# Optimization experiments

Hardware: AMD Instinct MI355X
Metric: run time of the kernel (lower is better)

The kernel has to match this reference:

```python
import jax, jax.numpy as jnp
import numpy as np

EPS = 1e-6
NUM_HEADS = 16
ROPE_THETA = 100000.0


def _rope_tables(seq_len, head_dim, theta):
    inv_freq = 1.0 / (theta ** (np.arange(0, head_dim, 2, dtype=np.float32) / head_dim))
    t = np.arange(seq_len, dtype=np.float32)
    freqs = np.outer(t, inv_freq)                      # (S, head_dim//2)
    emb = np.concatenate([freqs, freqs], axis=-1)      # (S, head_dim)
    return jnp.asarray(np.cos(emb))[None], jnp.asarray(np.sin(emb))[None]  # (1,S,D)


def setup_inputs() -> dict:
    key = jax.random.key(0)
    ks = jax.random.split(key, 6)
    B, S, H = 2, 2048, 1024
    head_dim = H // NUM_HEADS
    cos, sin = _rope_tables(S, head_dim, ROPE_THETA)
    scale = 0.02
    return {
        "hidden_states": jax.random.normal(ks[0], (B, S, H), dtype=jnp.float32),
        "cos": cos, "sin": sin,
        "Wq": jax.random.normal(ks[1], (H, H), dtype=jnp.float32) * scale,
        "bq": jnp.zeros((H,), dtype=jnp.float32),
        "Wk": jax.random.normal(ks[2], (H, H), dtype=jnp.float32) * scale,
        "bk": jnp.zeros((H,), dtype=jnp.float32),
        "Wv": jax.random.normal(ks[3], (H, H), dtype=jnp.float32) * scale,
        "bv": jnp.zeros((H,), dtype=jnp.float32),
        "Wo": jax.random.normal(ks[4], (H, H), dtype=jnp.float32) * scale,
        "bo": jnp.zeros((H,), dtype=jnp.float32),
        "rms_weight": jnp.ones((H,), dtype=jnp.float32),
    }


def _rms_norm(x, w):
    var = jnp.mean(x * x, axis=-1, keepdims=True)
    return x * jax.lax.rsqrt(var + EPS) * w


def _rotate_half(x):
    x1, x2 = jnp.split(x, 2, axis=-1)
    return jnp.concatenate([-x2, x1], axis=-1)


def reference(hidden_states, cos, sin, Wq, bq, Wk, bk, Wv, bv, Wo, bo, rms_weight):
    B, S, H = hidden_states.shape
    D = H // NUM_HEADS
    q = hidden_states @ Wq.T + bq
    k = hidden_states @ Wk.T + bk
    v = hidden_states @ Wv.T + bv
    # RMSNorm over full hidden dim BEFORE head split (as in original)
    q = _rms_norm(q, rms_weight)
    k = _rms_norm(k, rms_weight)
    # (B,S,H) -> (B,heads,S,D)
    q = q.reshape(B, S, NUM_HEADS, D).transpose(0, 2, 1, 3)
    k = k.reshape(B, S, NUM_HEADS, D).transpose(0, 2, 1, 3)
    v = v.reshape(B, S, NUM_HEADS, D).transpose(0, 2, 1, 3)
    # RoPE: cos/sin (1,S,D) -> unsqueeze head dim
    c = cos[:, None, :, :]
    s = sin[:, None, :, :]
    q = q * c + _rotate_half(q) * s
    k = k * c + _rotate_half(k) * s
    # attention (faithful: boolean tril mask is ADDED as 0/1, not -inf)
    scale = D ** 0.5
    scores = jnp.einsum("bhqd,bhkd->bhqk", q, k) / scale
    mask = jnp.tril(jnp.ones((S, S), dtype=scores.dtype))  # +1 on causal, +0 elsewhere
    attn = jax.nn.softmax(scores + mask, axis=-1)
    out = jnp.einsum("bhqk,bhkd->bhqd", attn, v)
    out = out.transpose(0, 2, 1, 3).reshape(B, S, H)
    return out @ Wo.T + bo
```

## Files before the change

kernel.cpp:

```cpp
#include <hip/hip_runtime.h>

typedef unsigned short u16;
typedef __attribute__((ext_vector_type(8))) short bf16x8;
typedef __attribute__((ext_vector_type(4))) short bf16x4;
typedef __attribute__((ext_vector_type(4))) float f32x4;

#define MFMA16(A,B,C) __builtin_amdgcn_mfma_f32_16x16x32_bf16(A,B,C,0,0,0)

__device__ __forceinline__ u16 f2bf(float f){
  unsigned int u; __builtin_memcpy(&u,&f,4);
  unsigned int r = (u + 0x7fffu + ((u>>16)&1u)) >> 16;
  return (u16)r;
}
__device__ __forceinline__ float bf2f(u16 h){
  unsigned int u = ((unsigned int)h) << 16;
  float f; __builtin_memcpy(&f,&u,4); return f;
}

__device__ __forceinline__ void async_ld16(const void* g, void* l) {
  __builtin_amdgcn_global_load_lds(
      (const __attribute__((address_space(1))) unsigned int*)g,
      (__attribute__((address_space(3))) unsigned int*)l, 16, 0, 0);
}

__global__ __launch_bounds__(256) void cast_all(const float* __restrict__ hs,
    const float* __restrict__ wq, const float* __restrict__ wk,
    const float* __restrict__ wv, const float* __restrict__ wo,
    u16* __restrict__ dst)
{
  unsigned int i = blockIdx.x*256 + threadIdx.x;
  size_t el = (size_t)i * 8;
  const float* src; size_t off;
  if (el < 4194304) { src = hs; off = el; }
  else {
    unsigned int r = (unsigned int)((el - 4194304) >> 20);
    src = (r==0)?wq:(r==1)?wk:(r==2)?wv:wo;
    off = (el - 4194304) & 1048575;
  }
  float4 a = *reinterpret_cast<const float4*>(src+off);
  float4 b = *reinterpret_cast<const float4*>(src+off+4);
  u16 tmp[8] = {f2bf(a.x),f2bf(a.y),f2bf(a.z),f2bf(a.w),
                f2bf(b.x),f2bf(b.y),f2bf(b.z),f2bf(b.w)};
  *reinterpret_cast<uint4*>(dst + el) = *reinterpret_cast<const uint4*>(tmp);
}

template<int MODE>
__global__ __launch_bounds__(256) void gemm_k(const u16* __restrict__ A,
                                              const u16* __restrict__ W,
                                              const float* __restrict__ b0p,
                                              const float* __restrict__ b1p,
                                              const float* __restrict__ b2p,
                                              void* __restrict__ out,
                                              int M, int N, int K)
{
  __shared__ __align__(16) u16 lds_a[128*32];
  __shared__ __align__(16) u16 lds_w[128*32];
  const int t = threadIdx.x;
  const int lane = t & 63, wave = t >> 6;
  const int wm = wave >> 1, wn = wave & 1;
  const int lr = lane & 15, quad = lane >> 4;
  const int n0 = blockIdx.x * 128, m0 = blockIdx.y * 128;
  const int wbase = t & 192;

  const f32x4 fzero = {0.f,0.f,0.f,0.f};
  f32x4 acc[4][4];
  #pragma unroll
  for (int i=0;i<4;++i)
    #pragma unroll
    for (int j=0;j<4;++j) acc[i][j] = fzero;

  for (int k0 = 0; k0 < K; k0 += 32) {
    __syncthreads();
    #pragma unroll
    for (int it=0; it<2; ++it) {
      int idx = it*256 + t;
      int row = idx >> 2, c8 = (idx & 3) * 8;
      int lbase = (it*256 + wbase) * 8;
      async_ld16(&A[(size_t)(m0+row)*K + k0 + c8], &lds_a[lbase]);
      async_ld16(&W[(size_t)(n0+row)*K + k0 + c8], &lds_w[lbase]);
    }
    __syncthreads();
    bf16x8 af[4], bfr[4];
    #pragma unroll
    for (int mt=0; mt<4; ++mt)
      af[mt] = *reinterpret_cast<const bf16x8*>(&lds_a[(wm*64 + mt*16 + lr)*32 + quad*8]);
    #pragma unroll
    for (int nt=0; nt<4; ++nt)
      bfr[nt] = *reinterpret_cast<const bf16x8*>(&lds_w[(wn*64 + nt*16 + lr)*32 + quad*8]);
    #pragma unroll
    for (int mt=0; mt<4; ++mt)
      #pragma unroll
      for (int nt=0; nt<4; ++nt)
        acc[mt][nt] = MFMA16(af[mt], bfr[nt], acc[mt][nt]);
  }

  if (MODE == 0) {
    float* O = reinterpret_cast<float*>(out);
    #pragma unroll
    for (int nt=0; nt<4; ++nt) {
      int n = n0 + wn*64 + nt*16 + lr;
      float bv = b0p[n];
      #pragma unroll
      for (int mt=0; mt<4; ++mt)
        #pragma unroll
        for (int r=0; r<4; ++r) {
          int m = m0 + wm*64 + mt*16 + quad*4 + r;
          O[(size_t)m * N + n] = acc[mt][nt][r] + bv;
        }
    }
  } else {
    int which = n0 >> 10;
    const float* bp = (which==0) ? b0p : (which==1) ? b1p : b2p;
    u16* dst = reinterpret_cast<u16*>(out) + (size_t)which * 4194304;
    if (which == 2) {
      #pragma unroll
      for (int nt=0; nt<4; ++nt) {
        int nn = (n0 & 1023) + wn*64 + nt*16 + lr;
        float bv = bp[nn];
        int hh = nn >> 6, d = nn & 63;
        #pragma unroll
        for (int mt=0; mt<4; ++mt) {
          int m = m0 + wm*64 + mt*16 + quad*4;
          int b = m >> 11, s = m & 2047;
          u16 o[4];
          #pragma unroll
          for (int r=0; r<4; ++r) o[r] = f2bf(acc[mt][nt][r] + bv);
          *reinterpret_cast<uint2*>(&dst[((size_t)(b*16 + hh)*64 + d)*2048 + s]) =
              *reinterpret_cast<const uint2*>(o);
        }
      }
    } else {
      #pragma unroll
      for (int nt=0; nt<4; ++nt) {
        int nn = (n0 & 1023) + wn*64 + nt*16 + lr;
        float bv = bp[nn];
        int hh = nn >> 6, d = nn & 63;
        #pragma unroll
        for (int mt=0; mt<4; ++mt)
          #pragma unroll
          for (int r=0; r<4; ++r) {
            int m = m0 + wm*64 + mt*16 + quad*4 + r;
            int b = m >> 11, s = m & 2047;
            dst[((size_t)(b*16 + hh) * 2048 + s) * 64 + d] = f2bf(acc[mt][nt][r] + bv);
          }
      }
    }
  }
}

__global__ __launch_bounds__(256) void rmsrope(u16* __restrict__ qb, u16* __restrict__ kb,
                                               const float* __restrict__ cosb,
                                               const float* __restrict__ sinb,
                                               const float* __restrict__ w)
{
  u16* buf = blockIdx.y ? kb : qb;
  const int bs = blockIdx.x;
  const int b = bs >> 11, s = bs & 2047;
  const int t = threadIdx.x;
  float x1[2], x2[2];
  float ss = 0.f;
  #pragma unroll
  for (int i=0;i<2;++i){
    int p = t + i*256;
    int h = p >> 5, d = p & 31;
    size_t base = ((size_t)(b*16+h)*2048 + s)*64;
    x1[i] = bf2f(buf[base + d]);
    x2[i] = bf2f(buf[base + d + 32]);
    ss += x1[i]*x1[i] + x2[i]*x2[i];
  }
  #pragma unroll
  for (int off=32; off>0; off>>=1) ss += __shfl_xor(ss, off, 64);
  __shared__ float red[4];
  if ((t & 63) == 0) red[t>>6] = ss;
  __syncthreads();
  float tot = red[0]+red[1]+red[2]+red[3];
  float r = rsqrtf(tot * (1.0f/1024.0f) + 1e-6f);
  #pragma unroll
  for (int i=0;i<2;++i){
    int p = t + i*256;
    int h = p >> 5, d = p & 31;
    size_t base = ((size_t)(b*16+h)*2048 + s)*64;
    float w1 = w[h*64+d], w2 = w[h*64+d+32];
    float n1 = x1[i]*r*w1, n2 = x2[i]*r*w2;
    float c1 = cosb[s*64+d],    s1 = sinb[s*64+d];
    float c2 = cosb[s*64+d+32], s2 = sinb[s*64+d+32];
    buf[base+d]    = f2bf(n1*c1 - n2*s1);
    buf[base+d+32] = f2bf(n2*c2 + n1*s2);
  }
}

__global__ __launch_bounds__(256) void attn(const u16* __restrict__ qh,
                                            const u16* __restrict__ kh,
                                            const u16* __restrict__ vt,
                                            u16* __restrict__ ao)
{
  __shared__ __align__(16) u16 kbuf[64*64];
  __shared__ __align__(16) u16 vbuf[64*64];
  const int t = threadIdx.x;
  const int lane = t & 63, w = t >> 6;
  const int lr = lane & 15, quad = lane >> 4;
  const int qbase = blockIdx.x * 64;
  const int bh = blockIdx.y;
  const int b = bh >> 4, h = bh & 15;
  const size_t hb = (size_t)bh * 2048 * 64;
  const u16* qp = qh + hb;
  const u16* kp = kh + hb;
  const u16* vtp = vt + hb;

  const int q_abs = qbase + w*16 + lr;
  bf16x8 qf0 = *reinterpret_cast<const bf16x8*>(&qp[(size_t)q_abs*64 + quad*8]);
  bf16x8 qf1 = *reinterpret_cast<const bf16x8*>(&qp[(size_t)q_abs*64 + 32 + quad*8]);

  const f32x4 fzero = {0.f,0.f,0.f,0.f};
  f32x4 oacc[4];
  #pragma unroll
  for (int i=0;i<4;++i) oacc[i] = fzero;
  float lsum = 0.f;

  for (int kt=0; kt<32; ++kt) {
    __syncthreads();
    #pragma unroll
    for (int it=0; it<2; ++it) {
      int idx = it*256 + t;
      int row = idx >> 3, c = idx & 7;
      uint4 kvv = *reinterpret_cast<const uint4*>(&kp[(size_t)(kt*64+row)*64 + c*8]);
      uint4 vvv = *reinterpret_cast<const uint4*>(&vtp[(size_t)row*2048 + kt*64 + c*8]);
      int sw = ((c ^ (row&7))&7)*8;
      *reinterpret_cast<uint4*>(&kbuf[row*64 + sw]) = kvv;
      *reinterpret_cast<uint4*>(&vbuf[row*64 + sw]) = vvv;
    }
    __syncthreads();

    bf16x8 pfr[2];
    #pragma unroll
    for (int u=0; u<2; ++u) {
      bf16x4 ph[2];
      #pragma unroll
      for (int sidx=0; sidx<2; ++sidx) {
        int ksub = u*2 + sidx;
        int row = ksub*16 + lr, sw = row & 7;
        bf16x8 a0 = *reinterpret_cast<const bf16x8*>(&kbuf[row*64 + ((quad ^ sw)&7)*8]);
        bf16x8 a1 = *reinterpret_cast<const bf16x8*>(&kbuf[row*64 + ((quad ^ sw ^ 4)&7)*8]);
        f32x4 z = fzero;
        z = MFMA16(a0, qf0, z);
        z = MFMA16(a1, qf1, z);
        int key0 = kt*64 + ksub*16 + quad*4;
        u16 pp[4];
        #pragma unroll
        for (int r=0; r<4; ++r) {
          float sc = z[r]*0.125f + ((key0 + r <= q_abs) ? 1.0f : 0.0f);
          float p = __expf(sc);
          lsum += p;
          pp[r] = f2bf(p);
        }
        __builtin_memcpy(&ph[sidx], pp, 8);
      }
      pfr[u] = __builtin_shufflevector(ph[0], ph[1], 0,1,2,3,4,5,6,7);
    }

    #pragma unroll
    for (int u=0; u<2; ++u) {
      #pragma unroll
      for (int dt=0; dt<4; ++dt) {
        int row = dt*16 + lr, sw = row & 7;
        int c0 = u*4 + (quad>>1);
        int io = (quad&1)*4;
        bf16x4 v0, v1;
        __builtin_memcpy(&v0, &vbuf[row*64 + ((c0 ^ sw)&7)*8 + io], 8);
        __builtin_memcpy(&v1, &vbuf[row*64 + (((c0+2) ^ sw)&7)*8 + io], 8);
        bf16x8 vf = __builtin_shufflevector(v0, v1, 0,1,2,3,4,5,6,7);
        oacc[dt] = MFMA16(vf, pfr[u], oacc[dt]);
      }
    }
  }

  lsum += __shfl_xor(lsum, 16, 64);
  lsum += __shfl_xor(lsum, 32, 64);
  float inv = 1.0f / lsum;
  size_t rowbase = ((size_t)(b*2048 + q_abs))*1024 + h*64;
  #pragma unroll
  for (int dt=0; dt<4; ++dt) {
    u16 o[4];
    #pragma unroll
    for (int r=0; r<4; ++r) o[r] = f2bf(oacc[dt][r] * inv);
    *reinterpret_cast<uint2*>(&ao[rowbase + dt*16 + quad*4]) =
        *reinterpret_cast<const uint2*>(o);
  }
}

extern "C" void kernel_launch(void* const* d_in, const int* in_sizes, int n_in,
                              void* d_out, int out_size, void* d_ws, size_t ws_size,
                              hipStream_t stream)
{
  const float* hs   = (const float*)d_in[0];
  const float* cosb = (const float*)d_in[1];
  const float* sinb = (const float*)d_in[2];
  const float* Wq   = (const float*)d_in[3];
  const float* bq   = (const float*)d_in[4];
  const float* Wk   = (const float*)d_in[5];
  const float* bk   = (const float*)d_in[6];
  const float* Wv   = (const float*)d_in[7];
  const float* bv   = (const float*)d_in[8];
  const float* Wo   = (const float*)d_in[9];
  const float* bo   = (const float*)d_in[10];
  const float* rw   = (const float*)d_in[11];

  const size_t NEL = (size_t)4096 * 1024;
  const size_t WEL = (size_t)1024 * 1024;
  u16* hsb = (u16*)d_ws;
  u16* wqb = hsb + NEL;
  u16* wob = wqb + 3*WEL;
  u16* qhb = wob + WEL;
  u16* khb = qhb + NEL;
  u16* vtb = khb + NEL;
  u16* aob = hsb;

  cast_all<<<4096, 256, 0, stream>>>(hs, Wq, Wk, Wv, Wo, hsb);
  gemm_k<1><<<dim3(24,32), 256, 0, stream>>>(hsb, wqb, bq, bk, bv, qhb, 4096, 3072, 1024);
  rmsrope<<<dim3(4096,2), 256, 0, stream>>>(qhb, khb, cosb, sinb, rw);
  attn<<<dim3(32,32), 256, 0, stream>>>(qhb, khb, vtb, aob);
  gemm_k<0><<<dim3(8,32), 256, 0, stream>>>(aob, wob, bo, nullptr, nullptr, d_out, 4096, 1024, 1024);
}
```

Before: 250.0 us.

## Retile output GEMM, pad attention LDS, use exp2 with block-level mask specialization

Splits the templated GEMM into a QKV kernel and a dedicated output-projection kernel with 128x64 tiles, doubling the grid from 256 to 512 blocks to better fill the GPU. The attention kernel replaces the XOR-swizzled LDS layout with 72-element padded rows and a permuted V store, so fragments load as single 16-byte reads. It also folds the scale and mask into an exp2 FMA and evaluates the per-element causal mask only on the diagonal tile. Results are packed to bf16 with a perm instruction. The padding raises LDS use, and the permuted V layout adds indexing complexity.

After: 235.2 us. 5.9% less time.

```diff
diff --git a/kernel.cpp b/kernel.cpp
--- a/kernel.cpp
+++ b/kernel.cpp
@@ -2,10 +2,11 @@
 
 typedef unsigned short u16;
 typedef __attribute__((ext_vector_type(8))) short bf16x8;
-typedef __attribute__((ext_vector_type(4))) short bf16x4;
 typedef __attribute__((ext_vector_type(4))) float f32x4;
 
 #define MFMA16(A,B,C) __builtin_amdgcn_mfma_f32_16x16x32_bf16(A,B,C,0,0,0)
+#define LOG2E 1.4426950408889634f
+#define C1 0.18033688011112042f
 
 __device__ __forceinline__ u16 f2bf(float f){
   unsigned int u; __builtin_memcpy(&u,&f,4);
@@ -15,6 +16,13 @@
 __device__ __forceinline__ float bf2f(u16 h){
   unsigned int u = ((unsigned int)h) << 16;
   float f; __builtin_memcpy(&f,&u,4); return f;
+}
+__device__ __forceinline__ unsigned int pack_bf16(float a, float b){
+  unsigned int ua, ub;
+  __builtin_memcpy(&ua,&a,4); __builtin_memcpy(&ub,&b,4);
+  ua = ua + 0x7fffu + ((ua>>16)&1u);
+  ub = ub + 0x7fffu + ((ub>>16)&1u);
+  return __builtin_amdgcn_perm(ub, ua, 0x07060302);
 }
 
 __device__ __forceinline__ void async_ld16(const void* g, void* l) {
@@ -44,14 +52,13 @@
   *reinterpret_cast<uint4*>(dst + el) = *reinterpret_cast<const uint4*>(tmp);
 }
 
-template<int MODE>
-__global__ __launch_bounds__(256) void gemm_k(const u16* __restrict__ A,
-                                              const u16* __restrict__ W,
-                                              const float* __restrict__ b0p,
-                                              const float* __restrict__ b1p,
-                                              const float* __restrict__ b2p,
-                                              void* __restrict__ out,
-                                              int M, int N, int K)
+__global__ __launch_bounds__(256) void gemm_qkv(const u16* __restrict__ A,
+                                                const u16* __restrict__ W,
+                                                const float* __restrict__ b0p,
+                                                const float* __restrict__ b1p,
+                                                const float* __restrict__ b2p,
+                                                u16* __restrict__ out,
+                                                int M, int N, int K)
 {
   __shared__ __align__(16) u16 lds_a[128*32];
   __shared__ __align__(16) u16 lds_w[128*32];
@@ -94,57 +101,101 @@
         acc[mt][nt] = MFMA16(af[mt], bfr[nt], acc[mt][nt]);
   }
 
-  if (MODE == 0) {
-    float* O = reinterpret_cast<float*>(out);
+  int which = n0 >> 10;
+  const float* bp = (which==0) ? b0p : (which==1) ? b1p : b2p;
+  u16* dst = out + (size_t)which * 4194304;
+  if (which == 2) {
     #pragma unroll
     for (int nt=0; nt<4; ++nt) {
-      int n = n0 + wn*64 + nt*16 + lr;
-      float bv = b0p[n];
+      int nn = (n0 & 1023) + wn*64 + nt*16 + lr;
+      float bv = bp[nn];
+      int hh = nn >> 6, d = nn & 63;
+      #pragma unroll
+      for (int mt=0; mt<4; ++mt) {
+        int m = m0 + wm*64 + mt*16 + quad*4;
+        int b = m >> 11, s = m & 2047;
+        u16 o[4];
+        #pragma unroll
+        for (int r=0; r<4; ++r) o[r] = f2bf(acc[mt][nt][r] + bv);
+        *reinterpret_cast<uint2*>(&dst[((size_t)(b*16 + hh)*64 + d)*2048 + s]) =
+            *reinterpret_cast<const uint2*>(o);
+      }
+    }
+  } else {
+    #pragma unroll
+    for (int nt=0; nt<4; ++nt) {
+      int nn = (n0 & 1023) + wn*64 + nt*16 + lr;
+      float bv = bp[nn];
+      int hh = nn >> 6, d = nn & 63;
       #pragma unroll
       for (int mt=0; mt<4; ++mt)
         #pragma unroll
         for (int r=0; r<4; ++r) {
           int m = m0 + wm*64 + mt*16 + quad*4 + r;
-          O[(size_t)m * N + n] = acc[mt][nt][r] + bv;
+          int b = m >> 11, s = m & 2047;
+          dst[((size_t)(b*16 + hh) * 2048 + s) * 64 + d] = f2bf(acc[mt][nt][r] + bv);
         }
     }
-  } else {
-    int which = n0 >> 10;
-    const float* bp = (which==0) ? b0p : (which==1) ? b1p : b2p;
-    u16* dst = reinterpret_cast<u16*>(out) + (size_t)which * 4194304;
-    if (which == 2) {
-      #pragma unroll
-      for (int nt=0; nt<4; ++nt) {
-        int nn = (n0 & 1023) + wn*64 + nt*16 + lr;
-        float bv = bp[nn];
-        int hh = nn >> 6, d = nn & 63;
-        #pragma unroll
-        for (int mt=0; mt<4; ++mt) {
-          int m = m0 + wm*64 + mt*16 + quad*4;
-          int b = m >> 11, s = m & 2047;
-          u16 o[4];
-          #pragma unroll
-          for (int r=0; r<4; ++r) o[r] = f2bf(acc[mt][nt][r] + bv);
-          *reinterpret_cast<uint2*>(&dst[((size_t)(b*16 + hh)*64 + d)*2048 + s]) =
-              *reinterpret_cast<const uint2*>(o);
-        }
+  }
+}
+
+__global__ __launch_bounds__(256) void gemm_o(const u16* __restrict__ A,
+                                              const u16* __restrict__ W,
+                                              const float* __restrict__ bias,
+                                              float* __restrict__ O,
+                                              int M, int N, int K)
+{
+  __shared__ __align__(16) u16 lds_a[128*32];
+  __shared__ __align__(16) u16 lds_w[64*32];
+  const int t = threadIdx.x;
+  const int lane = t & 63, wm = t >> 6;
+  const int lr = lane & 15, quad = lane >> 4;
+  const int n0 = blockIdx.x * 64, m0 = blockIdx.y * 128;
+  const int wbase = t & 192;
+
+  const f32x4 fzero = {0.f,0.f,0.f,0.f};
+  f32x4 acc[2][4];
+  #pragma unroll
+  for (int i=0;i<2;++i)
+    #pragma unroll
+    for (int j=0;j<4;++j) acc[i][j] = fzero;
+
+  for (int k0 = 0; k0 < K; k0 += 32) {
+    __syncthreads();
+    #pragma unroll
+    for (int it=0; it<2; ++it) {
+      int idx = it*256 + t;
+      int row = idx >> 2, c8 = (idx & 3) * 8;
+      int lbase = (it*256 + wbase) * 8;
+      async_ld16(&A[(size_t)(m0+row)*K + k0 + c8], &lds_a[lbase]);
+    }
+    async_ld16(&W[(size_t)(n0 + (t>>2))*K + k0 + (t&3)*8], &lds_w[wbase*8]);
+    __syncthreads();
+    bf16x8 af[2], bfr[4];
+    #pragma unroll
+    for (int mt=0; mt<2; ++mt)
+      af[mt] = *reinterpret_cast<const bf16x8*>(&lds_a[(wm*32 + mt*16 + lr)*32 + quad*8]);
+    #pragma unroll
+    for (int nt=0; nt<4; ++nt)
+      bfr[nt] = *reinterpret_cast<const bf16x8*>(&lds_w[(nt*16 + lr)*32 + quad*8]);
+    #pragma unroll
+    for (int mt=0; mt<2; ++mt)
+      #pragma unroll
+      for (int nt=0; nt<4; ++nt)
+        acc[mt][nt] = MFMA16(af[mt], bfr[nt], acc[mt][nt]);
+  }
+
+  #pragma unroll
+  for (int nt=0; nt<4; ++nt) {
+    int n = n0 + nt*16 + lr;
+    float bv = bias[n];
+    #pragma unroll
+    for (int mt=0; mt<2; ++mt)
+      #pragma unroll
+      for (int r=0; r<4; ++r) {
+        int m = m0 + wm*32 + mt*16 + quad*4 + r;
+        O[(size_t)m * N + n] = acc[mt][nt][r] + bv;
       }
-    } else {
-      #pragma unroll
-      for (int nt=0; nt<4; ++nt) {
-        int nn = (n0 & 1023) + wn*64 + nt*16 + lr;
-        float bv = bp[nn];
-        int hh = nn >> 6, d = nn & 63;
-        #pragma unroll
-        for (int mt=0; mt<4; ++mt)
-          #pragma unroll
-          for (int r=0; r<4; ++r) {
-            int m = m0 + wm*64 + mt*16 + quad*4 + r;
-            int b = m >> 11, s = m & 2047;
-            dst[((size_t)(b*16 + hh) * 2048 + s) * 64 + d] = f2bf(acc[mt][nt][r] + bv);
-          }
-      }
-    }
   }
 }
 
@@ -194,12 +245,13 @@
                                             const u16* __restrict__ vt,
                                             u16* __restrict__ ao)
 {
-  __shared__ __align__(16) u16 kbuf[64*64];
-  __shared__ __align__(16) u16 vbuf[64*64];
+  __shared__ __align__(16) u16 kbuf[64*72];
+  __shared__ __align__(16) u16 vbuf[64*72];
   const int t = threadIdx.x;
   const int lane = t & 63, w = t >> 6;
   const int lr = lane & 15, quad = lane >> 4;
-  const int qbase = blockIdx.x * 64;
+  const int bx = blockIdx.x;
+  const int qbase = bx * 64;
   const int bh = blockIdx.y;
   const int b = bh >> 4, h = bh & 15;
   const size_t hb = (size_t)bh * 2048 * 64;
@@ -211,65 +263,94 @@
   bf16x8 qf0 = *reinterpret_cast<const bf16x8*>(&qp[(size_t)q_abs*64 + quad*8]);
   bf16x8 qf1 = *reinterpret_cast<const bf16x8*>(&qp[(size_t)q_abs*64 + 32 + quad*8]);
 
+  const int row0 = t >> 3;
+  const int cc = t & 7;
+  const int c8 = cc * 8;
+  const int P0 = ((cc>>2)*32) + ((cc&1)*16) + (((cc>>1)&1)*4);
+  u16* kw0 = &kbuf[row0*72 + c8];
+  u16* kw1 = &kbuf[(row0+32)*72 + c8];
+  u16* vw0 = &vbuf[row0*72 + P0];
+  u16* vw1 = &vbuf[(row0+32)*72 + P0];
+
   const f32x4 fzero = {0.f,0.f,0.f,0.f};
   f32x4 oacc[4];
   #pragma unroll
   for (int i=0;i<4;++i) oacc[i] = fzero;
   float lsum = 0.f;
+  const int qoff = w*16 + lr;
 
   for (int kt=0; kt<32; ++kt) {
     __syncthreads();
-    #pragma unroll
-    for (int it=0; it<2; ++it) {
-      int idx = it*256 + t;
-      int row = idx >> 3, c = idx & 7;
-      uint4 kvv = *reinterpret_cast<const uint4*>(&kp[(size_t)(kt*64+row)*64 + c*8]);
-      uint4 vvv = *reinterpret_cast<const uint4*>(&vtp[(size_t)row*2048 + kt*64 + c*8]);
-      int sw = ((c ^ (row&7))&7)*8;
-      *reinterpret_cast<uint4*>(&kbuf[row*64 + sw]) = kvv;
-      *reinterpret_cast<uint4*>(&vbuf[row*64 + sw]) = vvv;
-    }
-    __syncthreads();
-
-    bf16x8 pfr[2];
-    #pragma unroll
-    for (int u=0; u<2; ++u) {
-      bf16x4 ph[2];
-      #pragma unroll
-      for (int sidx=0; sidx<2; ++sidx) {
-        int ksub = u*2 + sidx;
-        int row = ksub*16 + lr, sw = row & 7;
-        bf16x8 a0 = *reinterpret_cast<const bf16x8*>(&kbuf[row*64 + ((quad ^ sw)&7)*8]);
-        bf16x8 a1 = *reinterpret_cast<const bf16x8*>(&kbuf[row*64 + ((quad ^ sw ^ 4)&7)*8]);
-        f32x4 z = fzero;
-        z = MFMA16(a0, qf0, z);
-        z = MFMA16(a1, qf1, z);
-        int key0 = kt*64 + ksub*16 + quad*4;
-        u16 pp[4];
+    {
+      const u16* kg = kp + (size_t)kt*4096 + row0*64 + c8;
+      const u16* vg = vtp + (size_t)row0*2048 + kt*64 + c8;
+      uint4 k0 = *reinterpret_cast<const uint4*>(kg);
+      uint4 k1 = *reinterpret_cast<const uint4*>(kg + 32*64);
+      uint4 v0 = *reinterpret_cast<const uint4*>(vg);
+      uint4 v1 = *reinterpret_cast<const uint4*>(vg + 32*2048);
+      *reinterpret_cast<uint4*>(kw0) = k0;
+      *reinterpret_cast<uint4*>(kw1) = k1;
+      uint2 a0 = {v0.x, v0.y}, a1 = {v0.z, v0.w};
+      uint2 b0 = {v1.x, v1.y}, b1 = {v1.z, v1.w};
+      *reinterpret_cast<uint2*>(vw0)     = a0;
+      *reinterpret_cast<uint2*>(vw0 + 8) = a1;
+      *reinterpret_cast<uint2*>(vw1)     = b0;
+      *reinterpret_cast<uint2*>(vw1 + 8) = b1;
+    }
+    __syncthreads();
+
+    f32x4 zz[4];
+    #pragma unroll
+    for (int ksub=0; ksub<4; ++ksub) {
+      const u16* kr = &kbuf[(ksub*16+lr)*72 + quad*8];
+      bf16x8 a0, a1;
+      __builtin_memcpy(&a0, kr, 16);
+      __builtin_memcpy(&a1, kr+32, 16);
+      f32x4 z = fzero;
+      z = MFMA16(a0, qf0, z);
+      z = MFMA16(a1, qf1, z);
+      zz[ksub] = z;
+    }
+
+    unsigned int pk[4][2];
+    if (kt != bx) {
+      float ml = (kt < bx) ? LOG2E : 0.0f;
+      #pragma unroll
+      for (int ksub=0; ksub<4; ++ksub) {
+        float p0 = __builtin_amdgcn_exp2f(__builtin_fmaf(zz[ksub][0], C1, ml));
+        float p1 = __builtin_amdgcn_exp2f(__builtin_fmaf(zz[ksub][1], C1, ml));
+        float p2 = __builtin_amdgcn_exp2f(__builtin_fmaf(zz[ksub][2], C1, ml));
+        float p3 = __builtin_amdgcn_exp2f(__builtin_fmaf(zz[ksub][3], C1, ml));
+        lsum += (p0+p1) + (p2+p3);
+        pk[ksub][0] = pack_bf16(p0, p1);
+        pk[ksub][1] = pack_bf16(p2, p3);
+      }
+    } else {
+      #pragma unroll
+      for (int ksub=0; ksub<4; ++ksub) {
+        int koff = ksub*16 + quad*4;
+        float p[4];
         #pragma unroll
         for (int r=0; r<4; ++r) {
-          float sc = z[r]*0.125f + ((key0 + r <= q_abs) ? 1.0f : 0.0f);
-          float p = __expf(sc);
-          lsum += p;
-          pp[r] = f2bf(p);
+          float ml = (koff + r <= qoff) ? LOG2E : 0.0f;
+          p[r] = __builtin_amdgcn_exp2f(__builtin_fmaf(zz[ksub][r], C1, ml));
+          lsum += p[r];
         }
-        __builtin_memcpy(&ph[sidx], pp, 8);
+        pk[ksub][0] = pack_bf16(p[0], p[1]);
+        pk[ksub][1] = pack_bf16(p[2], p[3]);
       }
-      pfr[u] = __builtin_shufflevector(ph[0], ph[1], 0,1,2,3,4,5,6,7);
     }
 
     #pragma unroll
     for (int u=0; u<2; ++u) {
+      uint4 pq = {pk[2*u][0], pk[2*u][1], pk[2*u+1][0], pk[2*u+1][1]};
+      bf16x8 pf;
+      __builtin_memcpy(&pf, &pq, 16);
       #pragma unroll
       for (int dt=0; dt<4; ++dt) {
-        int row = dt*16 + lr, sw = row & 7;
-        int c0 = u*4 + (quad>>1);
-        int io = (quad&1)*4;
-        bf16x4 v0, v1;
-        __builtin_memcpy(&v0, &vbuf[row*64 + ((c0 ^ sw)&7)*8 + io], 8);
-        __builtin_memcpy(&v1, &vbuf[row*64 + (((c0+2) ^ sw)&7)*8 + io], 8);
-        bf16x8 vf = __builtin_shufflevector(v0, v1, 0,1,2,3,4,5,6,7);
-        oacc[dt] = MFMA16(vf, pfr[u], oacc[dt]);
+        bf16x8 vf;
+        __builtin_memcpy(&vf, &vbuf[(dt*16+lr)*72 + u*32 + quad*8], 16);
+        oacc[dt] = MFMA16(vf, pf, oacc[dt]);
       }
     }
   }
@@ -316,8 +397,8 @@
   u16* aob = hsb;
 
   cast_all<<<4096, 256, 0, stream>>>(hs, Wq, Wk, Wv, Wo, hsb);
-  gemm_k<1><<<dim3(24,32), 256, 0, stream>>>(hsb, wqb, bq, bk, bv, qhb, 4096, 3072, 1024);
+  gemm_qkv<<<dim3(24,32), 256, 0, stream>>>(hsb, wqb, bq, bk, bv, qhb, 4096, 3072, 1024);
   rmsrope<<<dim3(4096,2), 256, 0, stream>>>(qhb, khb, cosb, sinb, rw);
   attn<<<dim3(32,32), 256, 0, stream>>>(qhb, khb, vtb, aob);
-  gemm_k<0><<<dim3(8,32), 256, 0, stream>>>(aob, wob, bo, nullptr, nullptr, d_out, 4096, 1024, 1024);
-}
+  gemm_o<<<dim3(16,32), 256, 0, stream>>>(aob, wob, bo, (float*)d_out, 4096, 1024, 1024);
+}
```
